# Performance work log

Measured on AMD Instinct MI355X. Metric: run time of the kernel, lower is better.

The kernel has to match this reference:

```python
import jax, jax.numpy as jnp
import numpy as np

BETA = 1.0
DECAY = 0.95


def setup_inputs() -> dict:
    key = jax.random.key(0)
    ks = jax.random.split(key, 10)
    B, S, D = 8, 2048, 1024
    M, d = 4096, 256
    sc_in = 1.0 / np.sqrt(D)
    sc_slot = 1.0 / np.sqrt(d)
    return {
        "x": jax.random.normal(ks[0], (B, S, D), jnp.float32),
        "memory": jax.random.normal(ks[1], (B, M, d), jnp.float32) * 0.01,
        "Wq": jax.random.normal(ks[2], (D, d), jnp.float32) * sc_in,
        "bq": jnp.zeros((d,), jnp.float32),
        "Wv": jax.random.normal(ks[3], (D, d), jnp.float32) * sc_in,
        "bv": jnp.zeros((d,), jnp.float32),
        "Wo": jax.random.normal(ks[4], (d, D), jnp.float32) * sc_slot,
        "bo": jnp.zeros((D,), jnp.float32),
        "Wg": jax.random.normal(ks[5], (D, 1), jnp.float32) * sc_in,
        "bg": jnp.zeros((1,), jnp.float32),
    }


def reference(x, memory, Wq, bq, Wv, bv, Wo, bo, Wg, bg):
    # ---- shared summary + query ----
    x_summary = jnp.mean(x, axis=1)                      # [B, D]
    query = x_summary @ Wq + bq                          # [B, d]

    # ---- read: Hopfield retrieval against memory[0] (shared patterns) ----
    patterns = memory[0]                                 # [M, d]
    read_scores = BETA * (query @ patterns.T)            # [B, M]
    read_attn = jax.nn.softmax(read_scores, axis=-1)
    retrieved = read_attn @ patterns                     # [B, d]
    read_out = retrieved @ Wo + bo                       # [B, D]
    x_augmented = x + read_out[:, None, :]               # broadcast over seq

    # ---- write: gated EMA update to per-batch memory ----
    write_value = x_summary @ Wv + bv                    # [B, d]
    write_gate = jax.nn.sigmoid(x_summary @ Wg + bg)     # [B, 1]
    w_scores = BETA * jnp.einsum('bd,bmd->bm', query, memory)
    w_attn = jax.nn.softmax(w_scores, axis=-1)           # [B, M]
    update = write_gate[:, :, None] * write_value[:, None, :]   # [B, 1, d]
    weighted_update = w_attn[:, :, None] * update        # [B, M, d]
    memory_new = DECAY * memory + (1.0 - DECAY) * weighted_update

    return x_augmented, memory_new
```

## Files before the change

### kernel.cpp

```cpp
#include <hip/hip_runtime.h>
#include <math.h>

#define BB 8
#define SS 2048
#define DD 1024
#define MM 4096
#define dd 256
#define NCH 64
#define CS (SS/NCH)

#define OFF_PART  0
#define OFF_Q     524288
#define OFF_WV    526336
#define OFF_GATE  528384
#define OFF_COMBO 528392
#define OFF_SUMP  528400
#define OFF_SC    529424
#define OFF_PRET  562192
#define OFF_ROUT  693264

__global__ void k1(const float* __restrict__ x, float* __restrict__ ws) {
    int blk = blockIdx.x;
    int chunk = blk & 63;
    int b = blk >> 6;
    int t = threadIdx.x;
    const float4* x4 = (const float4*)(x + ((size_t)b*SS + (size_t)chunk*CS)*DD);
    float4 a = make_float4(0.f,0.f,0.f,0.f);
    #pragma unroll 8
    for (int s = 0; s < CS; ++s) {
        float4 v = x4[s*(DD/4) + t];
        a.x += v.x; a.y += v.y; a.z += v.z; a.w += v.w;
    }
    ((float4*)(ws + OFF_PART))[(size_t)(b*NCH + chunk)*256 + t] = a;
}

__global__ void k23(const float* __restrict__ Wq, const float* __restrict__ bq,
                    const float* __restrict__ Wv, const float* __restrict__ bv,
                    const float* __restrict__ Wg, const float* __restrict__ bg,
                    float* __restrict__ ws) {
    __shared__ float4 xsA[256];
    __shared__ float4 xsB[256];
    __shared__ float red[512];
    int blk = blockIdx.x;
    int t = threadIdx.x;
    const float4* p4 = (const float4*)(ws + OFF_PART);
    if (blk < 64) {
        int cs = blk & 3;
        int wb = blk >> 2;
        int b = wb & 7;
        int which = wb >> 3;
        int col4 = t & 255;
        int half = t >> 8;
        float4 a = make_float4(0.f,0.f,0.f,0.f);
        #pragma unroll 8
        for (int c = 0; c < 32; ++c) {
            float4 v = p4[(size_t)(b*NCH + half*32 + c)*256 + col4];
            a.x += v.x; a.y += v.y; a.z += v.z; a.w += v.w;
        }
        if (half == 0) xsA[col4] = a; else xsB[col4] = a;
        __syncthreads();
        if (t < 256) {
            float4 u = xsA[t], v = xsB[t];
            xsA[t] = make_float4((u.x+v.x)*(1.f/SS), (u.y+v.y)*(1.f/SS),
                                 (u.z+v.z)*(1.f/SS), (u.w+v.w)*(1.f/SS));
        }
        __syncthreads();
        const float* xs = (const float*)xsA;
        const float* W = which ? Wv : Wq;
        int kg = t >> 6;
        int c0 = cs*64 + (t & 63);
        float acc = 0.f;
        #pragma unroll 8
        for (int kk = 0; kk < 128; ++kk) {
            int k = kg*128 + kk;
            acc += xs[k] * W[(size_t)k*dd + c0];
        }
        red[t] = acc;
        __syncthreads();
        if (t < 64) {
            int c = cs*64 + t;
            float o = red[t] + red[t+64] + red[t+128] + red[t+192]
                    + red[t+256] + red[t+320] + red[t+384] + red[t+448];
            o += which ? bv[c] : bq[c];
            ws[(which ? OFF_WV : OFF_Q) + b*dd + c] = o;
        }
    } else {
        int b = blk - 64;
        const float* base = ws + OFF_PART + (size_t)(b*NCH)*DD;
        float wg0 = Wg[t], wg1 = Wg[t + 512];
        float acc = 0.f;
        #pragma unroll 8
        for (int c = 0; c < NCH; ++c) {
            const float* p = base + (size_t)c*DD;
            acc += p[t]*wg0 + p[t+512]*wg1;
        }
        red[t] = acc; __syncthreads();
        for (int s2 = 256; s2 > 0; s2 >>= 1) {
            if (t < s2) red[t] += red[t + s2];
            __syncthreads();
        }
        if (t == 0)
            ws[OFF_GATE + b] = 1.f / (1.f + __expf(-(red[0]*(1.f/SS) + bg[0])));
    }
}

__global__ void k45(const float* __restrict__ memory, float* __restrict__ ws) {
    __shared__ float esc[64];
    int idx = blockIdx.x;
    int which = idx >> 9;
    int b = (idx >> 6) & 7;
    int mc = idx & 63;
    int t = threadIdx.x;
    int wave = t >> 6, lane = t & 63;
    const float* tile = ((which == 0) ? memory : memory + (size_t)b*MM*dd)
                        + (size_t)mc*64*dd;
    const float4 qv = ((const float4*)(ws + OFF_Q + b*dd))[lane];
    #pragma unroll 4
    for (int i = 0; i < 16; ++i) {
        int r = i*4 + wave;
        float4 a = ((const float4*)(tile + (size_t)r*dd))[lane];
        float p = a.x*qv.x + a.y*qv.y + a.z*qv.z + a.w*qv.w;
        #pragma unroll
        for (int off = 32; off > 0; off >>= 1) p += __shfl_xor(p, off);
        if (lane == 0) esc[r] = __expf(p);
    }
    __syncthreads();
    if (t < 64) {
        float v = esc[t];
        #pragma unroll
        for (int off = 32; off > 0; off >>= 1) v += __shfl_xor(v, off);
        if (t == 0) ws[OFF_SUMP + which*512 + b*64 + mc] = v;
    }
    if (which == 0) {
        float acc = 0.f;
        #pragma unroll 8
        for (int i = 0; i < 64; ++i) acc += esc[i] * tile[(size_t)i*dd + t];
        ws[OFF_PRET + (size_t)(b*64 + mc)*dd + t] = acc;
    } else {
        if (t < 64) ws[OFF_SC + (size_t)b*MM + mc*64 + t] = esc[t];
    }
}

__global__ void k7(const float* __restrict__ Wo, const float* __restrict__ bo,
                   float* __restrict__ ws) {
    __shared__ float ret[dd];
    __shared__ float red[256];
    __shared__ float ssum;
    int blk = blockIdx.x;
    int cb = blk & 15;
    int b = blk >> 4;
    int t = threadIdx.x;
    if (t < 64) {
        float v = ws[OFF_SUMP + b*64 + t];
        #pragma unroll
        for (int off = 32; off > 0; off >>= 1) v += __shfl_xor(v, off);
        if (t == 0) ssum = v;
    } else if (t < 128 && cb == 0) {
        float v = ws[OFF_SUMP + 512 + b*64 + (t - 64)];
        #pragma unroll
        for (int off = 32; off > 0; off >>= 1) v += __shfl_xor(v, off);
        if (t == 64) ws[OFF_COMBO + b] = 0.05f * ws[OFF_GATE + b] / v;
    }
    float acc0 = 0.f;
    #pragma unroll 8
    for (int mc = 0; mc < 64; ++mc)
        acc0 += ws[OFF_PRET + (size_t)(b*64 + mc)*dd + t];
    __syncthreads();
    ret[t] = acc0 / ssum;
    __syncthreads();
    int c = t & 63, jr = t >> 6;
    float acc = 0.f;
    #pragma unroll 8
    for (int jj = 0; jj < 64; ++jj) {
        int j = jr*64 + jj;
        acc += ret[j] * Wo[(size_t)j*DD + cb*64 + c];
    }
    red[t] = acc; __syncthreads();
    if (t < 64) {
        ws[OFF_ROUT + (size_t)b*DD + cb*64 + t] =
            red[t] + red[t+64] + red[t+128] + red[t+192] + bo[cb*64 + t];
    }
}

__global__ void k8(const float* __restrict__ x, const float* __restrict__ memory,
                   const float* __restrict__ ws, float* __restrict__ out) {
    const int NA = BB*SS*DD/4;
    const int NT = NA + BB*MM*dd/4;
    const float4* x4 = (const float4*)x;
    const float4* m4 = (const float4*)memory;
    const float4* r4 = (const float4*)(ws + OFF_ROUT);
    const float4* w4 = (const float4*)(ws + OFF_WV);
    float4* o4 = (float4*)out;
    int stride = gridDim.x * blockDim.x;
    for (int i = blockIdx.x*blockDim.x + threadIdx.x; i < NT; i += stride) {
        if (i < NA) {
            int b = i >> 19;
            int c = i & 255;
            float4 xv = x4[i];
            float4 rv = r4[(b << 8) + c];
            o4[i] = make_float4(xv.x+rv.x, xv.y+rv.y, xv.z+rv.z, xv.w+rv.w);
        } else {
            int j = i - NA;
            int b = j >> 18;
            int m = (j >> 6) & (MM-1);
            int d4 = j & 63;
            float coeff = ws[OFF_COMBO + b] * ws[OFF_SC + (size_t)b*MM + m];
            float4 wv = w4[(b << 6) + d4];
            float4 mv = m4[j];
            o4[i] = make_float4(0.95f*mv.x + coeff*wv.x,
                                0.95f*mv.y + coeff*wv.y,
                                0.95f*mv.z + coeff*wv.z,
                                0.95f*mv.w + coeff*wv.w);
        }
    }
}

extern "C" void kernel_launch(void* const* d_in, const int* in_sizes, int n_in,
                              void* d_out, int out_size, void* d_ws, size_t ws_size,
                              hipStream_t stream) {
    const float* x      = (const float*)d_in[0];
    const float* memory = (const float*)d_in[1];
    const float* Wq     = (const float*)d_in[2];
    const float* bq     = (const float*)d_in[3];
    const float* Wv     = (const float*)d_in[4];
    const float* bv     = (const float*)d_in[5];
    const float* Wo     = (const float*)d_in[6];
    const float* bo     = (const float*)d_in[7];
    const float* Wg     = (const float*)d_in[8];
    const float* bg     = (const float*)d_in[9];
    float* out = (float*)d_out;
    float* ws  = (float*)d_ws;

    k1<<<BB*NCH, 256, 0, stream>>>(x, ws);
    k23<<<72, 512, 0, stream>>>(Wq, bq, Wv, bv, Wg, bg, ws);
    k45<<<1024, 256, 0, stream>>>(memory, ws);
    k7<<<BB*16, 256, 0, stream>>>(Wo, bo, ws);
    k8<<<4096, 256, 0, stream>>>(x, memory, ws, out);
}
```

Baseline: 73.80 us.

## Fuse five kernels into one persistent kernel with atomic grid barriers

Replaces the five separate launches with a single persistent kernel of 512 blocks that steps through the same stages, separated by a software grid barrier built on an atomic counter in the workspace. A memset before the launch zeroes the counter. The aim is to remove per-launch overhead and the idle gaps between dependent stages. It also changes the chunking of the sequence reduction (more, smaller chunks) and reshapes the projection and gate work. In exchange, the kernel depends on all 512 blocks being resident at once, and the final streaming pass now runs on far fewer threads than the old 4096-block elementwise kernel, which may lower achieved bandwidth.

```diff
diff --git a/kernel.cpp b/kernel.cpp
--- a/kernel.cpp
+++ b/kernel.cpp
@@ -6,211 +6,219 @@
 #define DD 1024
 #define MM 4096
 #define dd 256
-#define NCH 64
-#define CS (SS/NCH)
-
-#define OFF_PART  0
-#define OFF_Q     524288
-#define OFF_WV    526336
-#define OFF_GATE  528384
-#define OFF_COMBO 528392
-#define OFF_SUMP  528400
-#define OFF_SC    529424
-#define OFF_PRET  562192
-#define OFF_ROUT  693264
-
-__global__ void k1(const float* __restrict__ x, float* __restrict__ ws) {
-    int blk = blockIdx.x;
-    int chunk = blk & 63;
-    int b = blk >> 6;
-    int t = threadIdx.x;
-    const float4* x4 = (const float4*)(x + ((size_t)b*SS + (size_t)chunk*CS)*DD);
-    float4 a = make_float4(0.f,0.f,0.f,0.f);
-    #pragma unroll 8
-    for (int s = 0; s < CS; ++s) {
-        float4 v = x4[s*(DD/4) + t];
-        a.x += v.x; a.y += v.y; a.z += v.z; a.w += v.w;
-    }
-    ((float4*)(ws + OFF_PART))[(size_t)(b*NCH + chunk)*256 + t] = a;
+#define GRID 512
+#define NCHK 128
+
+#define OFF_PART  64
+#define OFF_Q     (OFF_PART + BB*NCHK*DD)
+#define OFF_WV    (OFF_Q + 2048)
+#define OFF_GATE  (OFF_WV + 2048)
+#define OFF_COMBO (OFF_GATE + 8)
+#define OFF_SUMP  (OFF_COMBO + 8)
+#define OFF_SC    (OFF_SUMP + 1024)
+#define OFF_PRET  (OFF_SC + 32768)
+#define OFF_ROUT  (OFF_PRET + 131072)
+
+__device__ __forceinline__ void gbar(int* cnt, int target) {
+    __syncthreads();
+    if (threadIdx.x == 0) {
+        __threadfence();
+        __hip_atomic_fetch_add(cnt, 1, __ATOMIC_RELAXED, __HIP_MEMORY_SCOPE_AGENT);
+        while (__hip_atomic_load(cnt, __ATOMIC_RELAXED, __HIP_MEMORY_SCOPE_AGENT) < target)
+            __builtin_amdgcn_s_sleep(8);
+        __threadfence();
+    }
+    __syncthreads();
 }
 
-__global__ void k23(const float* __restrict__ Wq, const float* __restrict__ bq,
-                    const float* __restrict__ Wv, const float* __restrict__ bv,
-                    const float* __restrict__ Wg, const float* __restrict__ bg,
-                    float* __restrict__ ws) {
-    __shared__ float4 xsA[256];
-    __shared__ float4 xsB[256];
-    __shared__ float red[512];
-    int blk = blockIdx.x;
-    int t = threadIdx.x;
-    const float4* p4 = (const float4*)(ws + OFF_PART);
-    if (blk < 64) {
-        int cs = blk & 3;
-        int wb = blk >> 2;
-        int b = wb & 7;
-        int which = wb >> 3;
-        int col4 = t & 255;
-        int half = t >> 8;
+__global__ __launch_bounds__(256, 4)
+void mega(const float* __restrict__ x, const float* __restrict__ memory,
+          const float* __restrict__ Wq, const float* __restrict__ bq,
+          const float* __restrict__ Wv, const float* __restrict__ bv,
+          const float* __restrict__ Wo, const float* __restrict__ bo,
+          const float* __restrict__ Wg, const float* __restrict__ bg,
+          float* __restrict__ ws, float* __restrict__ out) {
+    __shared__ float4 xs4[256];
+    __shared__ float red[256];
+    __shared__ float esc[64];
+    __shared__ float ret[256];
+    __shared__ float ssum;
+    const int blk = blockIdx.x;
+    const int t = threadIdx.x;
+    int* bar = (int*)ws;
+    float4* PART4 = (float4*)(ws + OFF_PART);
+
+    for (int u = blk; u < BB*NCHK; u += GRID) {
+        int b = u >> 7, chunk = u & 127;
+        const float4* x4 = (const float4*)(x + ((size_t)b*SS + (size_t)chunk*16)*DD);
         float4 a = make_float4(0.f,0.f,0.f,0.f);
-        #pragma unroll 8
-        for (int c = 0; c < 32; ++c) {
-            float4 v = p4[(size_t)(b*NCH + half*32 + c)*256 + col4];
+        #pragma unroll
+        for (int s = 0; s < 16; ++s) {
+            float4 v = x4[s*256 + t];
             a.x += v.x; a.y += v.y; a.z += v.z; a.w += v.w;
         }
-        if (half == 0) xsA[col4] = a; else xsB[col4] = a;
-        __syncthreads();
-        if (t < 256) {
-            float4 u = xsA[t], v = xsB[t];
-            xsA[t] = make_float4((u.x+v.x)*(1.f/SS), (u.y+v.y)*(1.f/SS),
-                                 (u.z+v.z)*(1.f/SS), (u.w+v.w)*(1.f/SS));
-        }
-        __syncthreads();
-        const float* xs = (const float*)xsA;
+        PART4[(size_t)u*256 + t] = a;
+    }
+    gbar(bar, GRID);
+
+    if (blk < 128) {
+        int which = blk >> 6;
+        int b = (blk >> 3) & 7;
+        int cgp = blk & 7;
+        const float4* p4 = PART4 + (size_t)b*NCHK*256;
+        float4 a = make_float4(0.f,0.f,0.f,0.f);
+        #pragma unroll 8
+        for (int c = 0; c < NCHK; ++c) {
+            float4 v = p4[(size_t)c*256 + t];
+            a.x += v.x; a.y += v.y; a.z += v.z; a.w += v.w;
+        }
+        xs4[t] = make_float4(a.x*(1.f/SS), a.y*(1.f/SS), a.z*(1.f/SS), a.w*(1.f/SS));
+        __syncthreads();
+        const float* xs = (const float*)xs4;
         const float* W = which ? Wv : Wq;
-        int kg = t >> 6;
-        int c0 = cs*64 + (t & 63);
+        int kg = t >> 5;
+        int c = cgp*32 + (t & 31);
         float acc = 0.f;
         #pragma unroll 8
         for (int kk = 0; kk < 128; ++kk) {
             int k = kg*128 + kk;
-            acc += xs[k] * W[(size_t)k*dd + c0];
+            acc += xs[k] * W[(size_t)k*dd + c];
         }
         red[t] = acc;
         __syncthreads();
-        if (t < 64) {
-            int c = cs*64 + t;
-            float o = red[t] + red[t+64] + red[t+128] + red[t+192]
-                    + red[t+256] + red[t+320] + red[t+384] + red[t+448];
-            o += which ? bv[c] : bq[c];
-            ws[(which ? OFF_WV : OFF_Q) + b*dd + c] = o;
-        }
-    } else {
-        int b = blk - 64;
-        const float* base = ws + OFF_PART + (size_t)(b*NCH)*DD;
-        float wg0 = Wg[t], wg1 = Wg[t + 512];
-        float acc = 0.f;
-        #pragma unroll 8
-        for (int c = 0; c < NCH; ++c) {
-            const float* p = base + (size_t)c*DD;
-            acc += p[t]*wg0 + p[t+512]*wg1;
-        }
-        red[t] = acc; __syncthreads();
-        for (int s2 = 256; s2 > 0; s2 >>= 1) {
+        if (t < 32) {
+            float o = 0.f;
+            #pragma unroll
+            for (int g = 0; g < 8; ++g) o += red[g*32 + t];
+            int cc = cgp*32 + t;
+            o += which ? bv[cc] : bq[cc];
+            ws[(which ? OFF_WV : OFF_Q) + b*dd + cc] = o;
+        }
+    } else if (blk < 136) {
+        int b = blk - 128;
+        const float4* p4 = PART4 + (size_t)b*NCHK*256;
+        float4 a = make_float4(0.f,0.f,0.f,0.f);
+        #pragma unroll 8
+        for (int c = 0; c < NCHK; ++c) {
+            float4 v = p4[(size_t)c*256 + t];
+            a.x += v.x; a.y += v.y; a.z += v.z; a.w += v.w;
+        }
+        float4 wg = ((const float4*)Wg)[t];
+        red[t] = a.x*wg.x + a.y*wg.y + a.z*wg.z + a.w*wg.w;
+        __syncthreads();
+        for (int s2 = 128; s2 > 0; s2 >>= 1) {
             if (t < s2) red[t] += red[t + s2];
             __syncthreads();
         }
         if (t == 0)
             ws[OFF_GATE + b] = 1.f / (1.f + __expf(-(red[0]*(1.f/SS) + bg[0])));
     }
-}
-
-__global__ void k45(const float* __restrict__ memory, float* __restrict__ ws) {
-    __shared__ float esc[64];
-    int idx = blockIdx.x;
-    int which = idx >> 9;
-    int b = (idx >> 6) & 7;
-    int mc = idx & 63;
-    int t = threadIdx.x;
-    int wave = t >> 6, lane = t & 63;
-    const float* tile = ((which == 0) ? memory : memory + (size_t)b*MM*dd)
-                        + (size_t)mc*64*dd;
-    const float4 qv = ((const float4*)(ws + OFF_Q + b*dd))[lane];
-    #pragma unroll 4
-    for (int i = 0; i < 16; ++i) {
-        int r = i*4 + wave;
-        float4 a = ((const float4*)(tile + (size_t)r*dd))[lane];
-        float p = a.x*qv.x + a.y*qv.y + a.z*qv.z + a.w*qv.w;
-        #pragma unroll
-        for (int off = 32; off > 0; off >>= 1) p += __shfl_xor(p, off);
-        if (lane == 0) esc[r] = __expf(p);
-    }
-    __syncthreads();
-    if (t < 64) {
-        float v = esc[t];
-        #pragma unroll
-        for (int off = 32; off > 0; off >>= 1) v += __shfl_xor(v, off);
-        if (t == 0) ws[OFF_SUMP + which*512 + b*64 + mc] = v;
-    }
-    if (which == 0) {
+    gbar(bar, 2*GRID);
+
+    {
+        int wave = t >> 6, lane = t & 63;
+        for (int u = blk; u < 1024; u += GRID) {
+            int which = u >> 9;
+            int b = (u >> 6) & 7;
+            int mc = u & 63;
+            const float* tile = ((which == 0) ? memory : memory + (size_t)b*MM*dd)
+                                + (size_t)mc*64*dd;
+            const float4 qv = ((const float4*)(ws + OFF_Q + b*dd))[lane];
+            #pragma unroll 4
+            for (int i = 0; i < 16; ++i) {
+                int r = i*4 + wave;
+                float4 av = ((const float4*)(tile + (size_t)r*dd))[lane];
+                float p = av.x*qv.x + av.y*qv.y + av.z*qv.z + av.w*qv.w;
+                #pragma unroll
+                for (int off = 32; off > 0; off >>= 1) p += __shfl_xor(p, off);
+                if (lane == 0) esc[r] = __expf(p);
+            }
+            __syncthreads();
+            if (t < 64) {
+                float v = esc[t];
+                #pragma unroll
+                for (int off = 32; off > 0; off >>= 1) v += __shfl_xor(v, off);
+                if (t == 0) ws[OFF_SUMP + which*512 + b*64 + mc] = v;
+            }
+            if (which == 0) {
+                float acc = 0.f;
+                #pragma unroll 8
+                for (int i = 0; i < 64; ++i) acc += esc[i] * tile[(size_t)i*dd + t];
+                ws[OFF_PRET + (size_t)(b*64 + mc)*dd + t] = acc;
+            } else if (t < 64) {
+                ws[OFF_SC + (size_t)b*MM + mc*64 + t] = esc[t];
+            }
+            __syncthreads();
+        }
+    }
+    gbar(bar, 3*GRID);
+
+    if (blk < 128) {
+        int cb = blk & 15;
+        int b = blk >> 4;
+        if (t < 64) {
+            float v = ws[OFF_SUMP + b*64 + t];
+            #pragma unroll
+            for (int off = 32; off > 0; off >>= 1) v += __shfl_xor(v, off);
+            if (t == 0) ssum = v;
+        } else if (t < 128 && cb == 0) {
+            float v = ws[OFF_SUMP + 512 + b*64 + (t - 64)];
+            #pragma unroll
+            for (int off = 32; off > 0; off >>= 1) v += __shfl_xor(v, off);
+            if (t == 64) ws[OFF_COMBO + b] = 0.05f * ws[OFF_GATE + b] / v;
+        }
+        float acc0 = 0.f;
+        #pragma unroll 8
+        for (int mc = 0; mc < 64; ++mc)
+            acc0 += ws[OFF_PRET + (size_t)(b*64 + mc)*dd + t];
+        __syncthreads();
+        ret[t] = acc0 / ssum;
+        __syncthreads();
+        int c = t & 63, jr = t >> 6;
         float acc = 0.f;
         #pragma unroll 8
-        for (int i = 0; i < 64; ++i) acc += esc[i] * tile[(size_t)i*dd + t];
-        ws[OFF_PRET + (size_t)(b*64 + mc)*dd + t] = acc;
-    } else {
-        if (t < 64) ws[OFF_SC + (size_t)b*MM + mc*64 + t] = esc[t];
-    }
-}
-
-__global__ void k7(const float* __restrict__ Wo, const float* __restrict__ bo,
-                   float* __restrict__ ws) {
-    __shared__ float ret[dd];
-    __shared__ float red[256];
-    __shared__ float ssum;
-    int blk = blockIdx.x;
-    int cb = blk & 15;
-    int b = blk >> 4;
-    int t = threadIdx.x;
-    if (t < 64) {
-        float v = ws[OFF_SUMP + b*64 + t];
-        #pragma unroll
-        for (int off = 32; off > 0; off >>= 1) v += __shfl_xor(v, off);
-        if (t == 0) ssum = v;
-    } else if (t < 128 && cb == 0) {
-        float v = ws[OFF_SUMP + 512 + b*64 + (t - 64)];
-        #pragma unroll
-        for (int off = 32; off > 0; off >>= 1) v += __shfl_xor(v, off);
-        if (t == 64) ws[OFF_COMBO + b] = 0.05f * ws[OFF_GATE + b] / v;
-    }
-    float acc0 = 0.f;
-    #pragma unroll 8
-    for (int mc = 0; mc < 64; ++mc)
-        acc0 += ws[OFF_PRET + (size_t)(b*64 + mc)*dd + t];
-    __syncthreads();
-    ret[t] = acc0 / ssum;
-    __syncthreads();
-    int c = t & 63, jr = t >> 6;
-    float acc = 0.f;
-    #pragma unroll 8
-    for (int jj = 0; jj < 64; ++jj) {
-        int j = jr*64 + jj;
-        acc += ret[j] * Wo[(size_t)j*DD + cb*64 + c];
-    }
-    red[t] = acc; __syncthreads();
-    if (t < 64) {
-        ws[OFF_ROUT + (size_t)b*DD + cb*64 + t] =
-            red[t] + red[t+64] + red[t+128] + red[t+192] + bo[cb*64 + t];
-    }
-}
-
-__global__ void k8(const float* __restrict__ x, const float* __restrict__ memory,
-                   const float* __restrict__ ws, float* __restrict__ out) {
-    const int NA = BB*SS*DD/4;
-    const int NT = NA + BB*MM*dd/4;
-    const float4* x4 = (const float4*)x;
-    const float4* m4 = (const float4*)memory;
-    const float4* r4 = (const float4*)(ws + OFF_ROUT);
-    const float4* w4 = (const float4*)(ws + OFF_WV);
-    float4* o4 = (float4*)out;
-    int stride = gridDim.x * blockDim.x;
-    for (int i = blockIdx.x*blockDim.x + threadIdx.x; i < NT; i += stride) {
-        if (i < NA) {
-            int b = i >> 19;
-            int c = i & 255;
-            float4 xv = x4[i];
-            float4 rv = r4[(b << 8) + c];
-            o4[i] = make_float4(xv.x+rv.x, xv.y+rv.y, xv.z+rv.z, xv.w+rv.w);
-        } else {
-            int j = i - NA;
-            int b = j >> 18;
-            int m = (j >> 6) & (MM-1);
-            int d4 = j & 63;
-            float coeff = ws[OFF_COMBO + b] * ws[OFF_SC + (size_t)b*MM + m];
-            float4 wv = w4[(b << 6) + d4];
-            float4 mv = m4[j];
-            o4[i] = make_float4(0.95f*mv.x + coeff*wv.x,
-                                0.95f*mv.y + coeff*wv.y,
-                                0.95f*mv.z + coeff*wv.z,
-                                0.95f*mv.w + coeff*wv.w);
+        for (int jj = 0; jj < 64; ++jj) {
+            int j = jr*64 + jj;
+            acc += ret[j] * Wo[(size_t)j*DD + cb*64 + c];
+        }
+        red[t] = acc;
+        __syncthreads();
+        if (t < 64) {
+            ws[OFF_ROUT + (size_t)b*DD + cb*64 + t] =
+                red[t] + red[t+64] + red[t+128] + red[t+192] + bo[cb*64 + t];
+        }
+    }
+    gbar(bar, 4*GRID);
+
+    {
+        const int NA = BB*SS*DD/4;
+        const int NT = NA + BB*MM*dd/4;
+        const float4* x4 = (const float4*)x;
+        const float4* m4 = (const float4*)memory;
+        const float4* r4 = (const float4*)(ws + OFF_ROUT);
+        const float4* w4 = (const float4*)(ws + OFF_WV);
+        float4* o4 = (float4*)out;
+        const int stride = GRID*256;
+        for (int i = blk*256 + t; i < NT; i += stride) {
+            if (i < NA) {
+                int b = i >> 19;
+                int c = i & 255;
+                float4 xv = x4[i];
+                float4 rv = r4[(b << 8) + c];
+                o4[i] = make_float4(xv.x+rv.x, xv.y+rv.y, xv.z+rv.z, xv.w+rv.w);
+            } else {
+                int j = i - NA;
+                int b = j >> 18;
+                int m = (j >> 6) & (MM-1);
+                int d4 = j & 63;
+                float coeff = ws[OFF_COMBO + b] * ws[OFF_SC + (size_t)b*MM + m];
+                float4 wv = w4[(b << 6) + d4];
+                float4 mv = m4[j];
+                o4[i] = make_float4(0.95f*mv.x + coeff*wv.x,
+                                    0.95f*mv.y + coeff*wv.y,
+                                    0.95f*mv.z + coeff*wv.z,
+                                    0.95f*mv.w + coeff*wv.w);
+            }
         }
     }
 }
@@ -231,9 +239,6 @@
     float* out = (float*)d_out;
     float* ws  = (float*)d_ws;
 
-    k1<<<BB*NCH, 256, 0, stream>>>(x, ws);
-    k23<<<72, 512, 0, stream>>>(Wq, bq, Wv, bv, Wg, bg, ws);
-    k45<<<1024, 256, 0, stream>>>(memory, ws);
-    k7<<<BB*16, 256, 0, stream>>>(Wo, bo, ws);
-    k8<<<4096, 256, 0, stream>>>(x, memory, ws, out);
+    hipMemsetAsync(ws, 0, 256, stream);
+    mega<<<GRID, 256, 0, stream>>>(x, memory, Wq, bq, Wv, bv, Wo, bo, Wg, bg, ws, out);
 }
```

Result: slower. 245.2 us (+232.3%).

## Fuse read-out projection into scoring kernel via last-block counter; add nontemporal streaming

Applied to the files above, without the earlier changes.

Merges the separate read-out kernel into the memory-scoring kernel. Each block bumps a per-batch atomic counter, and the last block of each batch reduces the softmax sums, computes the combo coefficient and does the full Wo projection. The counters are zeroed in the earlier kernel. Separately, the x and memory streams in the summary and final elementwise kernels use nontemporal loads and stores, and the summary pass splits into 128 chunks instead of 64. This removes one kernel launch and its sync point and eases cache pollution. The cost is serialising the Wo GEMV onto one block per batch, which may add a tail.

```diff
diff --git a/kernel.cpp b/kernel.cpp
--- a/kernel.cpp
+++ b/kernel.cpp
@@ -6,44 +6,44 @@
 #define DD 1024
 #define MM 4096
 #define dd 256
-#define NCH 64
-#define CS (SS/NCH)
-
-#define OFF_PART  0
-#define OFF_Q     524288
-#define OFF_WV    526336
-#define OFF_GATE  528384
-#define OFF_COMBO 528392
-#define OFF_SUMP  528400
-#define OFF_SC    529424
-#define OFF_PRET  562192
-#define OFF_ROUT  693264
+#define NCHK 128
+
+typedef float f4 __attribute__((ext_vector_type(4)));
+
+#define OFF_PART  64
+#define OFF_Q     (OFF_PART + BB*NCHK*DD)
+#define OFF_WV    (OFF_Q + 2048)
+#define OFF_GATE  (OFF_WV + 2048)
+#define OFF_COMBO (OFF_GATE + 8)
+#define OFF_SUMP  (OFF_COMBO + 8)
+#define OFF_SC    (OFF_SUMP + 1024)
+#define OFF_PRET  (OFF_SC + 32768)
+#define OFF_ROUT  (OFF_PRET + 131072)
 
 __global__ void k1(const float* __restrict__ x, float* __restrict__ ws) {
     int blk = blockIdx.x;
-    int chunk = blk & 63;
-    int b = blk >> 6;
+    int chunk = blk & 127;
+    int b = blk >> 7;
     int t = threadIdx.x;
-    const float4* x4 = (const float4*)(x + ((size_t)b*SS + (size_t)chunk*CS)*DD);
-    float4 a = make_float4(0.f,0.f,0.f,0.f);
-    #pragma unroll 8
-    for (int s = 0; s < CS; ++s) {
-        float4 v = x4[s*(DD/4) + t];
-        a.x += v.x; a.y += v.y; a.z += v.z; a.w += v.w;
-    }
-    ((float4*)(ws + OFF_PART))[(size_t)(b*NCH + chunk)*256 + t] = a;
+    const f4* x4 = (const f4*)(x + ((size_t)b*SS + (size_t)chunk*16)*DD);
+    f4 a = (f4)(0.f);
+    #pragma unroll
+    for (int s = 0; s < 16; ++s)
+        a += __builtin_nontemporal_load(&x4[s*256 + t]);
+    ((f4*)(ws + OFF_PART))[(size_t)blk*256 + t] = a;
 }
 
 __global__ void k23(const float* __restrict__ Wq, const float* __restrict__ bq,
                     const float* __restrict__ Wv, const float* __restrict__ bv,
                     const float* __restrict__ Wg, const float* __restrict__ bg,
                     float* __restrict__ ws) {
-    __shared__ float4 xsA[256];
-    __shared__ float4 xsB[256];
+    __shared__ f4 xsA[256];
+    __shared__ f4 xsB[256];
     __shared__ float red[512];
     int blk = blockIdx.x;
     int t = threadIdx.x;
-    const float4* p4 = (const float4*)(ws + OFF_PART);
+    const f4* p4 = (const f4*)(ws + OFF_PART);
+    if (blk == 71 && t < 8) ((int*)ws)[t] = 0;
     if (blk < 64) {
         int cs = blk & 3;
         int wb = blk >> 2;
@@ -51,19 +51,13 @@
         int which = wb >> 3;
         int col4 = t & 255;
         int half = t >> 8;
-        float4 a = make_float4(0.f,0.f,0.f,0.f);
-        #pragma unroll 8
-        for (int c = 0; c < 32; ++c) {
-            float4 v = p4[(size_t)(b*NCH + half*32 + c)*256 + col4];
-            a.x += v.x; a.y += v.y; a.z += v.z; a.w += v.w;
-        }
+        f4 a = (f4)(0.f);
+        #pragma unroll 8
+        for (int c = 0; c < 64; ++c)
+            a += p4[(size_t)(b*NCHK + half*64 + c)*256 + col4];
         if (half == 0) xsA[col4] = a; else xsB[col4] = a;
         __syncthreads();
-        if (t < 256) {
-            float4 u = xsA[t], v = xsB[t];
-            xsA[t] = make_float4((u.x+v.x)*(1.f/SS), (u.y+v.y)*(1.f/SS),
-                                 (u.z+v.z)*(1.f/SS), (u.w+v.w)*(1.f/SS));
-        }
+        if (t < 256) xsA[t] = (xsA[t] + xsB[t]) * (1.f/SS);
         __syncthreads();
         const float* xs = (const float*)xsA;
         const float* W = which ? Wv : Wq;
@@ -86,11 +80,11 @@
         }
     } else {
         int b = blk - 64;
-        const float* base = ws + OFF_PART + (size_t)(b*NCH)*DD;
+        const float* base = ws + OFF_PART + (size_t)(b*NCHK)*DD;
         float wg0 = Wg[t], wg1 = Wg[t + 512];
         float acc = 0.f;
         #pragma unroll 8
-        for (int c = 0; c < NCH; ++c) {
+        for (int c = 0; c < NCHK; ++c) {
             const float* p = base + (size_t)c*DD;
             acc += p[t]*wg0 + p[t+512]*wg1;
         }
@@ -104,22 +98,28 @@
     }
 }
 
-__global__ void k45(const float* __restrict__ memory, float* __restrict__ ws) {
+__global__ void k45f(const float* __restrict__ memory,
+                     const float* __restrict__ Wo, const float* __restrict__ bo,
+                     float* ws) {
     __shared__ float esc[64];
-    int idx = blockIdx.x;
-    int which = idx >> 9;
-    int b = (idx >> 6) & 7;
-    int mc = idx & 63;
+    __shared__ float ret[dd];
+    __shared__ float sS, sW;
+    __shared__ int lflag;
+    int blk = blockIdx.x;
+    int which = blk >> 9;
+    int b = (blk >> 6) & 7;
+    int mc = blk & 63;
     int t = threadIdx.x;
     int wave = t >> 6, lane = t & 63;
     const float* tile = ((which == 0) ? memory : memory + (size_t)b*MM*dd)
                         + (size_t)mc*64*dd;
-    const float4 qv = ((const float4*)(ws + OFF_Q + b*dd))[lane];
+    const f4 qv = ((const f4*)(ws + OFF_Q + b*dd))[lane];
     #pragma unroll 4
     for (int i = 0; i < 16; ++i) {
         int r = i*4 + wave;
-        float4 a = ((const float4*)(tile + (size_t)r*dd))[lane];
-        float p = a.x*qv.x + a.y*qv.y + a.z*qv.z + a.w*qv.w;
+        f4 av = ((const f4*)(tile + (size_t)r*dd))[lane];
+        f4 pr = av * qv;
+        float p = pr.x + pr.y + pr.z + pr.w;
         #pragma unroll
         for (int off = 32; off > 0; off >>= 1) p += __shfl_xor(p, off);
         if (lane == 0) esc[r] = __expf(p);
@@ -129,56 +129,58 @@
         float v = esc[t];
         #pragma unroll
         for (int off = 32; off > 0; off >>= 1) v += __shfl_xor(v, off);
-        if (t == 0) ws[OFF_SUMP + which*512 + b*64 + mc] = v;
+        if (t == 0)
+            __hip_atomic_store(ws + OFF_SUMP + which*512 + b*64 + mc, v,
+                               __ATOMIC_RELAXED, __HIP_MEMORY_SCOPE_AGENT);
     }
     if (which == 0) {
         float acc = 0.f;
         #pragma unroll 8
         for (int i = 0; i < 64; ++i) acc += esc[i] * tile[(size_t)i*dd + t];
-        ws[OFF_PRET + (size_t)(b*64 + mc)*dd + t] = acc;
-    } else {
-        if (t < 64) ws[OFF_SC + (size_t)b*MM + mc*64 + t] = esc[t];
-    }
-}
-
-__global__ void k7(const float* __restrict__ Wo, const float* __restrict__ bo,
-                   float* __restrict__ ws) {
-    __shared__ float ret[dd];
-    __shared__ float red[256];
-    __shared__ float ssum;
-    int blk = blockIdx.x;
-    int cb = blk & 15;
-    int b = blk >> 4;
-    int t = threadIdx.x;
+        __hip_atomic_store(ws + OFF_PRET + (size_t)(b*64 + mc)*dd + t, acc,
+                           __ATOMIC_RELAXED, __HIP_MEMORY_SCOPE_AGENT);
+    } else if (t < 64) {
+        ws[OFF_SC + (size_t)b*MM + mc*64 + t] = esc[t];
+    }
+    asm volatile("s_waitcnt vmcnt(0)" ::: "memory");
+    __syncthreads();
+    if (t == 0) {
+        int prev = __hip_atomic_fetch_add((int*)ws + b, 1,
+                                          __ATOMIC_RELAXED, __HIP_MEMORY_SCOPE_AGENT);
+        lflag = (prev == 127);
+    }
+    __syncthreads();
+    if (!lflag) return;
+    float v0 = 0.f, v1 = 0.f;
     if (t < 64) {
-        float v = ws[OFF_SUMP + b*64 + t];
+        v0 = __hip_atomic_load(ws + OFF_SUMP + b*64 + t,
+                               __ATOMIC_RELAXED, __HIP_MEMORY_SCOPE_AGENT);
+        v1 = __hip_atomic_load(ws + OFF_SUMP + 512 + b*64 + t,
+                               __ATOMIC_RELAXED, __HIP_MEMORY_SCOPE_AGENT);
         #pragma unroll
-        for (int off = 32; off > 0; off >>= 1) v += __shfl_xor(v, off);
-        if (t == 0) ssum = v;
-    } else if (t < 128 && cb == 0) {
-        float v = ws[OFF_SUMP + 512 + b*64 + (t - 64)];
-        #pragma unroll
-        for (int off = 32; off > 0; off >>= 1) v += __shfl_xor(v, off);
-        if (t == 64) ws[OFF_COMBO + b] = 0.05f * ws[OFF_GATE + b] / v;
-    }
+        for (int off = 32; off > 0; off >>= 1) {
+            v0 += __shfl_xor(v0, off);
+            v1 += __shfl_xor(v1, off);
+        }
+        if (t == 0) { sS = v0; sW = v1; }
+    }
+    __syncthreads();
+    if (t == 0) ws[OFF_COMBO + b] = 0.05f * ws[OFF_GATE + b] / sW;
     float acc0 = 0.f;
     #pragma unroll 8
-    for (int mc = 0; mc < 64; ++mc)
-        acc0 += ws[OFF_PRET + (size_t)(b*64 + mc)*dd + t];
-    __syncthreads();
-    ret[t] = acc0 / ssum;
-    __syncthreads();
-    int c = t & 63, jr = t >> 6;
-    float acc = 0.f;
-    #pragma unroll 8
-    for (int jj = 0; jj < 64; ++jj) {
-        int j = jr*64 + jj;
-        acc += ret[j] * Wo[(size_t)j*DD + cb*64 + c];
-    }
-    red[t] = acc; __syncthreads();
-    if (t < 64) {
-        ws[OFF_ROUT + (size_t)b*DD + cb*64 + t] =
-            red[t] + red[t+64] + red[t+128] + red[t+192] + bo[cb*64 + t];
+    for (int m2 = 0; m2 < 64; ++m2)
+        acc0 += __hip_atomic_load(ws + OFF_PRET + (size_t)(b*64 + m2)*dd + t,
+                                  __ATOMIC_RELAXED, __HIP_MEMORY_SCOPE_AGENT);
+    ret[t] = acc0 / sS;
+    __syncthreads();
+    #pragma unroll
+    for (int cg = 0; cg < 4; ++cg) {
+        int col = cg*256 + t;
+        float acc = 0.f;
+        #pragma unroll 8
+        for (int j = 0; j < dd; ++j)
+            acc += ret[j] * Wo[(size_t)j*DD + col];
+        ws[OFF_ROUT + (size_t)b*DD + col] = acc + bo[col];
     }
 }
 
@@ -186,31 +188,29 @@
                    const float* __restrict__ ws, float* __restrict__ out) {
     const int NA = BB*SS*DD/4;
     const int NT = NA + BB*MM*dd/4;
-    const float4* x4 = (const float4*)x;
-    const float4* m4 = (const float4*)memory;
-    const float4* r4 = (const float4*)(ws + OFF_ROUT);
-    const float4* w4 = (const float4*)(ws + OFF_WV);
-    float4* o4 = (float4*)out;
+    const f4* x4 = (const f4*)x;
+    const f4* m4 = (const f4*)memory;
+    const f4* r4 = (const f4*)(ws + OFF_ROUT);
+    const f4* w4 = (const f4*)(ws + OFF_WV);
+    f4* o4 = (f4*)out;
     int stride = gridDim.x * blockDim.x;
     for (int i = blockIdx.x*blockDim.x + threadIdx.x; i < NT; i += stride) {
         if (i < NA) {
             int b = i >> 19;
             int c = i & 255;
-            float4 xv = x4[i];
-            float4 rv = r4[(b << 8) + c];
-            o4[i] = make_float4(xv.x+rv.x, xv.y+rv.y, xv.z+rv.z, xv.w+rv.w);
+            f4 xv = __builtin_nontemporal_load(&x4[i]);
+            f4 o = xv + r4[(b << 8) + c];
+            __builtin_nontemporal_store(o, &o4[i]);
         } else {
             int j = i - NA;
             int b = j >> 18;
             int m = (j >> 6) & (MM-1);
             int d4 = j & 63;
             float coeff = ws[OFF_COMBO + b] * ws[OFF_SC + (size_t)b*MM + m];
-            float4 wv = w4[(b << 6) + d4];
-            float4 mv = m4[j];
-            o4[i] = make_float4(0.95f*mv.x + coeff*wv.x,
-                                0.95f*mv.y + coeff*wv.y,
-                                0.95f*mv.z + coeff*wv.z,
-                                0.95f*mv.w + coeff*wv.w);
+            f4 wv = w4[(b << 6) + d4];
+            f4 mv = __builtin_nontemporal_load(&m4[j]);
+            f4 o = 0.95f*mv + coeff*wv;
+            __builtin_nontemporal_store(o, &o4[i]);
         }
     }
 }
@@ -231,9 +231,8 @@
     float* out = (float*)d_out;
     float* ws  = (float*)d_ws;
 
-    k1<<<BB*NCH, 256, 0, stream>>>(x, ws);
+    k1<<<BB*NCHK, 256, 0, stream>>>(x, ws);
     k23<<<72, 512, 0, stream>>>(Wq, bq, Wv, bv, Wg, bg, ws);
-    k45<<<1024, 256, 0, stream>>>(memory, ws);
-    k7<<<BB*16, 256, 0, stream>>>(Wo, bo, ws);
+    k45f<<<1024, 256, 0, stream>>>(memory, Wo, bo, ws);
     k8<<<4096, 256, 0, stream>>>(x, memory, ws, out);
 }
```

Measured after the change: 139.6 us. 89.2% more time.
